# Performance work log

Hardware: AMD Instinct MI355X
Metric: run time of the kernel (lower is better)

Reference implementation:

```python
import jax, jax.numpy as jnp
import numpy as np

S, D_MODEL, H, D_K, D_V = 2048, 1024, 16, 64, 64


def setup_inputs() -> dict:
    key = jax.random.key(0)
    ks = jax.random.split(key, 10)
    sd = 0.02
    return {
        "embeddings": jax.random.normal(ks[0], (S, D_MODEL), dtype=jnp.float32),
        # per-head projection weights (torch Linear: y = x @ W.T + b; here stored as [h, d_in, d_out])
        "Wq": jax.random.normal(ks[1], (H, D_MODEL, D_K), dtype=jnp.float32) * sd,
        "bq": jax.random.normal(ks[2], (H, D_K), dtype=jnp.float32) * sd,
        "Wk": jax.random.normal(ks[3], (H, D_MODEL, D_K), dtype=jnp.float32) * sd,
        "bk": jax.random.normal(ks[4], (H, D_K), dtype=jnp.float32) * sd,
        "Wv": jax.random.normal(ks[5], (H, D_MODEL, D_V), dtype=jnp.float32) * sd,
        "bv": jax.random.normal(ks[6], (H, D_V), dtype=jnp.float32) * sd,
        "Wo": jax.random.normal(ks[7], (H * D_V, D_MODEL), dtype=jnp.float32) * sd,
        "bo": jax.random.normal(ks[8], (D_MODEL,), dtype=jnp.float32) * sd,
    }


def reference(embeddings, Wq, bq, Wk, bk, Wv, bv, Wo, bo):
    # Batched equivalent of the per-head Python loop of ScaledDotProductAttention layers.
    # q,k: [h, s, d_k]; v: [h, s, d_v]
    q = jnp.einsum('sd,hdk->hsk', embeddings, Wq) + bq[:, None, :]
    k = jnp.einsum('sd,hdk->hsk', embeddings, Wk) + bk[:, None, :]
    v = jnp.einsum('sd,hdv->hsv', embeddings, Wv) + bv[:, None, :]
    scale = jnp.asarray(1.0 / np.sqrt(q.shape[-1]), q.dtype)
    scores = jnp.einsum('hsk,htk->hst', q, k) * scale  # [h, s, s]
    attn = jax.nn.softmax(scores, axis=-1)
    heads = jnp.einsum('hst,htv->hsv', attn, v)  # [h, s, d_v]
    # torch.cat(results, dim=1): head outputs concatenated along feature dim -> [s, h*d_v]
    concat = jnp.transpose(heads, (1, 0, 2)).reshape(embeddings.shape[0], -1)
    return concat @ Wo + bo
```

## Files before the change

### kernel.cpp

```cpp
#include <hip/hip_runtime.h>
#include <hip/hip_bf16.h>

typedef unsigned short u16;
typedef __attribute__((ext_vector_type(8))) short bf16x8;
typedef __attribute__((ext_vector_type(4))) float f32x4;
typedef __attribute__((ext_vector_type(16))) float f32x16;

#define S_LEN 2048
#define NH 16

__device__ __forceinline__ u16 f2bf(float x) {
  union { float f; unsigned u; } v; v.f = x;
  unsigned r = v.u + 0x7fffu + ((v.u >> 16) & 1u);
  return (u16)(r >> 16);
}

__device__ __forceinline__ unsigned cvtpk_bf16(float lo, float hi) {
  unsigned w;
  asm("v_cvt_pk_bf16_f32 %0, %1, %2" : "=v"(w) : "v"(lo), "v"(hi));
  return w;
}

__device__ __forceinline__ void plswap(unsigned& a, unsigned& b) {
  asm volatile("v_permlane32_swap_b32 %0, %1" : "+v"(a), "+v"(b));
}

__device__ __forceinline__ float fexp2(float x) {
#if __has_builtin(__builtin_amdgcn_exp2f)
  return __builtin_amdgcn_exp2f(x);
#else
  float y;
  asm volatile("v_exp_f32 %0, %1\n\ts_nop 0" : "=v"(y) : "v"(x));
  return y;
#endif
}

__device__ __forceinline__ void async16(const void* g, void* l) {
  __builtin_amdgcn_global_load_lds(
      (const __attribute__((address_space(1))) unsigned int*)g,
      (__attribute__((address_space(3))) unsigned int*)l, 16, 0, 0);
}

__device__ __forceinline__ f32x4 mfma16(bf16x8 a, bf16x8 b, f32x4 c) {
  return __builtin_amdgcn_mfma_f32_16x16x32_bf16(a, b, c, 0, 0, 0);
}
__device__ __forceinline__ f32x16 mfma32(bf16x8 a, bf16x8 b, f32x16 c) {
  return __builtin_amdgcn_mfma_f32_32x32x16_bf16(a, b, c, 0, 0, 0);
}

#define QSCALE (0.125f * 1.44269504089f)

__global__ __launch_bounds__(256) void convert_kernel(
    const float* __restrict__ emb, const float* __restrict__ Wq,
    const float* __restrict__ Wk, const float* __restrict__ Wv,
    const float* __restrict__ bq, const float* __restrict__ bk,
    const float* __restrict__ bv, const float* __restrict__ Wo,
    u16* __restrict__ emb_bf, u16* __restrict__ wqkv_t,
    u16* __restrict__ wo_t, float* __restrict__ bqkv) {
  __shared__ float lds[64][65];
  const int b = blockIdx.x, tid = threadIdx.x;
  if (b < 2048) {
    int i = b * 1024 + tid * 4;
    float4 v = *(const float4*)(emb + i);
    ushort4 o = {f2bf(v.x), f2bf(v.y), f2bf(v.z), f2bf(v.w)};
    *(ushort4*)(emb_bf + i) = o;
    return;
  }
  if (b < 2816) {
    int tt = b - 2048;
    int kind = tt >> 8;
    int rem = tt & 255;
    int h = rem >> 4, k0 = (rem & 15) << 6;
    const float* W = (kind == 0) ? Wq : ((kind == 1) ? Wk : Wv);
    const float* src = W + ((size_t)h * 1024 + k0) * 64;
#pragma unroll
    for (int rr = 0; rr < 4; ++rr) {
      int k = rr * 16 + (tid >> 4);
      int d4 = (tid & 15) << 2;
      float4 v = *(const float4*)(src + (size_t)k * 64 + d4);
      lds[k][d4] = v.x; lds[k][d4 + 1] = v.y;
      lds[k][d4 + 2] = v.z; lds[k][d4 + 3] = v.w;
    }
    __syncthreads();
    float scale = (kind == 0) ? QSCALE : 1.f;
#pragma unroll
    for (int p = 0; p < 2; ++p) {
      int d = p * 32 + (tid >> 3);
      int kb = (tid & 7) << 3;
      bf16x8 o;
#pragma unroll
      for (int j = 0; j < 8; ++j) o[j] = (short)f2bf(lds[kb + j][d] * scale);
      *(bf16x8*)(wqkv_t + (size_t)(kind * 1024 + h * 64 + d) * 1024 + k0 + kb) = o;
    }
    return;
  }
  if (b < 3072) {
    int tt = b - 2816;
    int k0 = (tt >> 4) << 6, n0 = (tt & 15) << 6;
#pragma unroll
    for (int rr = 0; rr < 4; ++rr) {
      int k = rr * 16 + (tid >> 4);
      int n4 = (tid & 15) << 2;
      float4 v = *(const float4*)(Wo + (size_t)(k0 + k) * 1024 + n0 + n4);
      lds[k][n4] = v.x; lds[k][n4 + 1] = v.y;
      lds[k][n4 + 2] = v.z; lds[k][n4 + 3] = v.w;
    }
    __syncthreads();
#pragma unroll
    for (int p = 0; p < 2; ++p) {
      int nrel = p * 32 + (tid >> 3);
      int kb = (tid & 7) << 3;
      bf16x8 o;
#pragma unroll
      for (int j = 0; j < 8; ++j) o[j] = (short)f2bf(lds[kb + j][nrel]);
      *(bf16x8*)(wo_t + (size_t)(n0 + nrel) * 1024 + k0 + kb) = o;
    }
    return;
  }
  for (int i = tid; i < 3072; i += 256) {
    int kind = i >> 10, hd = i & 1023;
    const float* bb = (kind == 0) ? bq : ((kind == 1) ? bk : bv);
    float v = bb[hd];
    bqkv[i] = (kind == 0) ? v * QSCALE : v;
  }
}

template <int WM, int WN, int FM, int FN, int BK, bool OUT_BF16, bool SPLIT>
__global__ __launch_bounds__(WM * WN * 64) void gemm_kernel(
    const u16* __restrict__ A, const u16* __restrict__ BT,
    const float* __restrict__ bias, void* __restrict__ Cout,
    u16* __restrict__ kp, u16* __restrict__ vp, int M, int N, int K) {
  constexpr int BM = WM * FM * 16, BN = WN * FN * 16, T = WM * WN * 64;
  constexpr int RB = BK * 2;
  __shared__ u16 lds[2][(BM + BN) * BK];
  const int tid = threadIdx.x;
  const int lane = tid & 63, wave = tid >> 6;
  const int wr = wave / WN, wc = wave % WN;
  const int m0 = blockIdx.x * BM, n0 = blockIdx.y * BN;
  const int r = lane & 15, g = lane >> 4;
  const f32x4 fzero = {0.f, 0.f, 0.f, 0.f};
  f32x4 acc[FM][FN];
#pragma unroll
  for (int i = 0; i < FM; ++i)
#pragma unroll
    for (int j = 0; j < FN; ++j) acc[i][j] = fzero;

  constexpr int LA = (BM * RB) / (T * 16);
  constexpr int LB = (BN * RB) / (T * 16);

  auto stage = [&](int kt, int buf) {
    int k0 = kt * BK;
#pragma unroll
    for (int i = 0; i < LA; ++i) {
      int flat = i * T * 16 + tid * 16;
      int row = flat / RB, colb = flat % RB;
      async16((const char*)A + ((size_t)(m0 + row) * K + k0) * 2 + colb,
              (char*)lds[buf] + i * T * 16 + wave * 1024);
    }
#pragma unroll
    for (int i = 0; i < LB; ++i) {
      int flat = i * T * 16 + tid * 16;
      int row = flat / RB, colb = flat % RB;
      async16((const char*)BT + ((size_t)(n0 + row) * K + k0) * 2 + colb,
              (char*)lds[buf] + BM * RB + i * T * 16 + wave * 1024);
    }
  };

  stage(0, 0);
  asm volatile("s_waitcnt vmcnt(0)" ::: "memory");
  __syncthreads();

  const int NT = K / BK;
  for (int kt = 0; kt < NT; ++kt) {
    int cur = kt & 1;
    if (kt + 1 < NT) stage(kt + 1, cur ^ 1);
    const u16* Al = lds[cur];
    const u16* Bl = Al + BM * BK;
#pragma unroll
    for (int kk = 0; kk < BK / 32; ++kk) {
      bf16x8 af[FM], bfr[FN];
#pragma unroll
      for (int i = 0; i < FM; ++i)
        af[i] = *(const bf16x8*)&Al[(wr * FM * 16 + i * 16 + r) * BK + kk * 32 + g * 8];
#pragma unroll
      for (int j = 0; j < FN; ++j)
        bfr[j] = *(const bf16x8*)&Bl[(wc * FN * 16 + j * 16 + r) * BK + kk * 32 + g * 8];
#pragma unroll
      for (int i = 0; i < FM; ++i)
#pragma unroll
        for (int j = 0; j < FN; ++j)
          acc[i][j] = mfma16(af[i], bfr[j], acc[i][j]);
    }
    asm volatile("s_waitcnt vmcnt(0)" ::: "memory");
    __syncthreads();
  }

  if constexpr (SPLIT) {
    if (n0 >= 2048) {
#pragma unroll
      for (int i = 0; i < FM; ++i)
#pragma unroll
        for (int j = 0; j < FN; ++j) {
          int d = wc * FN * 16 + j * 16 + r;
          int hd = n0 - 2048 + d;
          int h = hd >> 6, dd = hd & 63;
          u16* base = vp + (size_t)h * 131072;
          int t0v = m0 + wr * FM * 16 + i * 16 + g * 4;
          float bval = bias[n0 + d];
          int off = (t0v >> 6) * 4096 + ((((t0v >> 4) & 3) * 2 + (dd >> 5))) * 512 +
                    ((dd & 31) * 2 + ((t0v >> 3) & 1)) * 8 + (t0v & 7);
          ushort4 o = {f2bf(acc[i][j][0] + bval), f2bf(acc[i][j][1] + bval),
                       f2bf(acc[i][j][2] + bval), f2bf(acc[i][j][3] + bval)};
          *(ushort4*)(base + off) = o;
        }
      return;
    }
    if (n0 >= 1024) {
#pragma unroll
      for (int i = 0; i < FM; ++i)
#pragma unroll
        for (int j = 0; j < FN; ++j) {
          int d = wc * FN * 16 + j * 16 + r;
          int hd = n0 - 1024 + d;
          int h = hd >> 6, dd = hd & 63;
          u16* base = kp + (size_t)h * 131072;
          float bval = bias[n0 + d];
#pragma unroll
          for (int e = 0; e < 4; ++e) {
            int t = m0 + wr * FM * 16 + i * 16 + g * 4 + e;
            int off = (t >> 5) * 2048 + (dd >> 4) * 512 +
                      ((t & 31) * 2 + ((dd >> 3) & 1)) * 8 + (dd & 7);
            base[off] = f2bf(acc[i][j][e] + bval);
          }
        }
      return;
    }
#pragma unroll
    for (int i = 0; i < FM; ++i)
#pragma unroll
      for (int j = 0; j < FN; ++j)
#pragma unroll
        for (int e = 0; e < 4; ++e) {
          int row = m0 + wr * FM * 16 + i * 16 + g * 4 + e;
          int col = n0 + wc * FN * 16 + j * 16 + r;
          ((u16*)Cout)[(size_t)row * 1024 + col] = f2bf(acc[i][j][e] + bias[col]);
        }
    return;
  }

#pragma unroll
  for (int i = 0; i < FM; ++i)
#pragma unroll
    for (int j = 0; j < FN; ++j)
#pragma unroll
      for (int e = 0; e < 4; ++e) {
        int row = m0 + wr * FM * 16 + i * 16 + g * 4 + e;
        int col = n0 + wc * FN * 16 + j * 16 + r;
        float v = acc[i][j][e] + bias[col];
        if constexpr (OUT_BF16)
          ((u16*)Cout)[(size_t)row * N + col] = f2bf(v);
        else
          ((float*)Cout)[(size_t)row * N + col] = v;
      }
}

__global__ __launch_bounds__(256, 1) void attn_kernel(const u16* __restrict__ qbuf,
                                                      const u16* __restrict__ kp,
                                                      const u16* __restrict__ vp,
                                                      u16* __restrict__ concat) {
  const int tid = threadIdx.x, lane = tid & 63, wave = tid >> 6;
  const int swz = (blockIdx.x & 7) * 32 + (blockIdx.x >> 3);
  const int h = swz >> 4, qg = swz & 15;
  const int q0w = qg * 128 + wave * 32;
  const int l31 = lane & 31, hi5 = lane >> 5;
  const char* kb = (const char*)kp + (size_t)h * 262144;
  const char* vb = (const char*)vp + (size_t)h * 262144;
  const int loff = (l31 * 2 + hi5) * 16;

  bf16x8 qf[4];
#pragma unroll
  for (int ds = 0; ds < 4; ++ds)
    qf[ds] = *(const bf16x8*)&qbuf[(size_t)(q0w + l31) * 1024 + h * 64 + ds * 16 + hi5 * 8];

  f32x16 acc0 = {}, acc1 = {};
  float rs = 0.f;

  bf16x8 kA[8], kB[8];
#pragma unroll
  for (int i = 0; i < 8; ++i) kA[i] = *(const bf16x8*)(kb + i * 1024 + loff);

  auto stepf = [&](int t, bf16x8(&kc)[8], bf16x8(&kn)[8]) {
    __builtin_amdgcn_s_barrier();
    bf16x8 vF[8];
    const char* vbase = vb + (size_t)t * 8192;
#pragma unroll
    for (int i = 0; i < 8; ++i) vF[i] = *(const bf16x8*)(vbase + i * 1024 + loff);
    const char* knb = kb + (size_t)(t + 1) * 8192;
#pragma unroll
    for (int i = 0; i < 8; ++i) kn[i] = *(const bf16x8*)(knb + i * 1024 + loff);

    f32x16 sv0 = {}, sv1 = {};
    __builtin_amdgcn_s_setprio(1);
#pragma unroll
    for (int ds = 0; ds < 4; ++ds) {
      sv0 = mfma32(kc[ds], qf[ds], sv0);
      sv1 = mfma32(kc[4 + ds], qf[ds], sv1);
    }
    __builtin_amdgcn_s_setprio(0);

    bf16x8 pa[4];
#pragma unroll
    for (int s = 0; s < 2; ++s) {
      float e[16];
#pragma unroll
      for (int c = 0; c < 16; ++c) {
        e[c] = fexp2(s == 0 ? sv0[c] : sv1[c]);
        rs += e[c];
      }
      unsigned u0 = cvtpk_bf16(e[0], e[1]), v0 = cvtpk_bf16(e[2], e[3]);
      unsigned w0 = cvtpk_bf16(e[4], e[5]), z0 = cvtpk_bf16(e[6], e[7]);
      plswap(u0, w0);
      plswap(v0, z0);
      uint4 pk0 = {u0, v0, w0, z0};
      pa[2 * s] = *(bf16x8*)&pk0;
      unsigned u1 = cvtpk_bf16(e[8], e[9]), v1 = cvtpk_bf16(e[10], e[11]);
      unsigned w1 = cvtpk_bf16(e[12], e[13]), z1 = cvtpk_bf16(e[14], e[15]);
      plswap(u1, w1);
      plswap(v1, z1);
      uint4 pk1 = {u1, v1, w1, z1};
      pa[2 * s + 1] = *(bf16x8*)&pk1;
    }

    __builtin_amdgcn_s_setprio(1);
#pragma unroll
    for (int tsl = 0; tsl < 4; ++tsl) {
      acc0 = mfma32(pa[tsl], vF[tsl * 2 + 0], acc0);
      acc1 = mfma32(pa[tsl], vF[tsl * 2 + 1], acc1);
    }
    __builtin_amdgcn_s_setprio(0);
  };

  for (int t = 0; t < 32; t += 2) {
    stepf(t, kA, kB);
    stepf(t + 1, kB, kA);
  }

  rs += __shfl_xor(rs, 32, 64);

#pragma unroll
  for (int c = 0; c < 16; ++c) {
    int q = (c & 3) + 8 * (c >> 2) + 4 * hi5;
    float dn = __shfl(rs, q, 64);
    float inv = 1.f / dn;
    size_t rowb = (size_t)(q0w + q) * 1024 + h * 64;
    concat[rowb + l31] = f2bf(acc0[c] * inv);
    concat[rowb + 32 + l31] = f2bf(acc1[c] * inv);
  }
}

extern "C" void kernel_launch(void* const* d_in, const int* in_sizes, int n_in,
                              void* d_out, int out_size, void* d_ws,
                              size_t ws_size, hipStream_t stream) {
  (void)in_sizes; (void)n_in; (void)out_size; (void)ws_size;
  const float* emb = (const float*)d_in[0];
  const float* Wq = (const float*)d_in[1];
  const float* bq = (const float*)d_in[2];
  const float* Wk = (const float*)d_in[3];
  const float* bk = (const float*)d_in[4];
  const float* Wv = (const float*)d_in[5];
  const float* bv = (const float*)d_in[6];
  const float* Wo = (const float*)d_in[7];
  const float* bo = (const float*)d_in[8];

  char* ws = (char*)d_ws;
  u16* emb_bf  = (u16*)(ws + 0);
  u16* wqkv_t  = (u16*)(ws + 4194304);
  u16* wo_t    = (u16*)(ws + 10485760);
  float* bqkv  = (float*)(ws + 12582912);
  u16* qbuf    = (u16*)(ws + 12595200);
  u16* kpack   = (u16*)(ws + 16789504);
  u16* vpack   = (u16*)(ws + 20983808);
  u16* concat  = (u16*)(ws + 29372416);

  convert_kernel<<<3073, 256, 0, stream>>>(emb, Wq, Wk, Wv, bq, bk, bv, Wo,
                                           emb_bf, wqkv_t, wo_t, bqkv);
  gemm_kernel<2, 2, 4, 4, 32, true, true><<<dim3(16, 24), 256, 0, stream>>>(
      emb_bf, wqkv_t, bqkv, qbuf, kpack, vpack, 2048, 3072, 1024);
  attn_kernel<<<256, 256, 0, stream>>>(qbuf, kpack, vpack, concat);
  gemm_kernel<2, 2, 2, 2, 64, false, false><<<dim3(32, 16), 256, 0, stream>>>(
      concat, wo_t, bo, d_out, nullptr, nullptr, 2048, 1024, 1024);
}
```

Before: 81.26 us.

## Stage K/V tiles through LDS with a four-deep async global-to-LDS pipeline

Attention K and V tiles were loaded straight from global memory into registers by every wave, with a double-buffered K prefetch. They are now copied cooperatively into a four-slot LDS ring with async global_load_lds, prefetched three tiles ahead and synchronised with vmcnt waits plus barriers. Each tile is fetched from global once per block instead of once per wave, and the loads overlap compute. In exchange it adds 64KB of LDS, extra LDS reads and a barrier per tile.

```diff
diff --git a/kernel.cpp b/kernel.cpp
--- a/kernel.cpp
+++ b/kernel.cpp
@@ -39,6 +39,11 @@
   __builtin_amdgcn_global_load_lds(
       (const __attribute__((address_space(1))) unsigned int*)g,
       (__attribute__((address_space(3))) unsigned int*)l, 16, 0, 0);
+}
+
+template <int N>
+__device__ __forceinline__ void vmwait() {
+  asm volatile("s_waitcnt vmcnt(%0)" ::"i"(N) : "memory");
 }
 
 __device__ __forceinline__ f32x4 mfma16(bf16x8 a, bf16x8 b, f32x4 c) {
@@ -268,6 +273,7 @@
                                                       const u16* __restrict__ kp,
                                                       const u16* __restrict__ vp,
                                                       u16* __restrict__ concat) {
+  __shared__ __align__(16) char smem[4][16384];
   const int tid = threadIdx.x, lane = tid & 63, wave = tid >> 6;
   const int swz = (blockIdx.x & 7) * 32 + (blockIdx.x >> 3);
   const int h = swz >> 4, qg = swz & 15;
@@ -285,26 +291,37 @@
   f32x16 acc0 = {}, acc1 = {};
   float rs = 0.f;
 
-  bf16x8 kA[8], kB[8];
-#pragma unroll
-  for (int i = 0; i < 8; ++i) kA[i] = *(const bf16x8*)(kb + i * 1024 + loff);
-
-  auto stepf = [&](int t, bf16x8(&kc)[8], bf16x8(&kn)[8]) {
-    __builtin_amdgcn_s_barrier();
-    bf16x8 vF[8];
-    const char* vbase = vb + (size_t)t * 8192;
-#pragma unroll
-    for (int i = 0; i < 8; ++i) vF[i] = *(const bf16x8*)(vbase + i * 1024 + loff);
-    const char* knb = kb + (size_t)(t + 1) * 8192;
-#pragma unroll
-    for (int i = 0; i < 8; ++i) kn[i] = *(const bf16x8*)(knb + i * 1024 + loff);
+  auto stage = [&](int t) {
+    char* dst = smem[t & 3] + tid * 16;
+    const char* ksrc = kb + (size_t)t * 8192 + tid * 16;
+    const char* vsrc = vb + (size_t)t * 8192 + tid * 16;
+    async16(ksrc, dst);
+    async16(ksrc + 4096, dst + 4096);
+    async16(vsrc, dst + 8192);
+    async16(vsrc + 4096, dst + 12288);
+  };
+
+  constexpr int NT = 32;
+  stage(0);
+  stage(1);
+  stage(2);
+  vmwait<8>();
+  __builtin_amdgcn_s_barrier();
+  __builtin_amdgcn_sched_barrier(0);
+
+  for (int t = 0; t < NT; ++t) {
+    if (t + 3 < NT) stage(t + 3);
+    const char* Kb = smem[t & 3];
+    const char* Vb = Kb + 8192;
 
     f32x16 sv0 = {}, sv1 = {};
     __builtin_amdgcn_s_setprio(1);
 #pragma unroll
     for (int ds = 0; ds < 4; ++ds) {
-      sv0 = mfma32(kc[ds], qf[ds], sv0);
-      sv1 = mfma32(kc[4 + ds], qf[ds], sv1);
+      const bf16x8 k0 = *(const bf16x8*)(Kb + ds * 1024 + loff);
+      const bf16x8 k1 = *(const bf16x8*)(Kb + (4 + ds) * 1024 + loff);
+      sv0 = mfma32(k0, qf[ds], sv0);
+      sv1 = mfma32(k1, qf[ds], sv1);
     }
     __builtin_amdgcn_s_setprio(0);
 
@@ -334,15 +351,20 @@
     __builtin_amdgcn_s_setprio(1);
 #pragma unroll
     for (int tsl = 0; tsl < 4; ++tsl) {
-      acc0 = mfma32(pa[tsl], vF[tsl * 2 + 0], acc0);
-      acc1 = mfma32(pa[tsl], vF[tsl * 2 + 1], acc1);
+      const bf16x8 v0 = *(const bf16x8*)(Vb + (tsl * 2 + 0) * 1024 + loff);
+      const bf16x8 v1 = *(const bf16x8*)(Vb + (tsl * 2 + 1) * 1024 + loff);
+      acc0 = mfma32(pa[tsl], v0, acc0);
+      acc1 = mfma32(pa[tsl], v1, acc1);
     }
     __builtin_amdgcn_s_setprio(0);
-  };
-
-  for (int t = 0; t < 32; t += 2) {
-    stepf(t, kA, kB);
-    stepf(t + 1, kB, kA);
+
+    if (t + 1 < NT) {
+      if (t + 3 < NT) vmwait<8>();
+      else if (t + 2 < NT) vmwait<4>();
+      else vmwait<0>();
+      __builtin_amdgcn_s_barrier();
+      __builtin_amdgcn_sched_barrier(0);
+    }
   }
 
   rs += __shfl_xor(rs, 32, 64);
```

Result: no change. 81.49 us (+0.3%).
